# Performance work log

Measured on AMD Instinct MI355X. Metric: run time of the kernel, lower is better.

The kernel has to match this reference:

```python
import jax, jax.numpy as jnp
import numpy as np

DIM = 1024
HEADS = 16
NUM_EXPERTS = 8
TOP_K = 2
INNER = 4 * DIM
EPS = 1e-5
NEG = -1e9


def setup_inputs() -> dict:
    key = jax.random.key(0)
    ks = jax.random.split(key, 12)
    s = 0.02
    return {
        "x": jax.random.normal(ks[0], (4, 1024, DIM), dtype=jnp.float32),
        "qkv_w": jax.random.normal(ks[1], (DIM, 3 * DIM), dtype=jnp.float32) * s,
        "out_w": jax.random.normal(ks[2], (DIM, DIM), dtype=jnp.float32) * s,
        "out_b": jnp.zeros((DIM,), dtype=jnp.float32),
        "thresh": jnp.float32(-2.0),
        "ln1_g": jnp.ones((DIM,), dtype=jnp.float32),
        "ln1_b": jnp.zeros((DIM,), dtype=jnp.float32),
        "ln2_g": jnp.ones((DIM,), dtype=jnp.float32),
        "ln2_b": jnp.zeros((DIM,), dtype=jnp.float32),
        "gate_w": jax.random.normal(ks[3], (DIM, NUM_EXPERTS), dtype=jnp.float32) * s,
        "w1": jax.random.normal(ks[4], (NUM_EXPERTS, DIM, INNER), dtype=jnp.float32) * s,
        "b1": jnp.zeros((NUM_EXPERTS, INNER), dtype=jnp.float32),
        "w2": jax.random.normal(ks[5], (NUM_EXPERTS, INNER, DIM), dtype=jnp.float32) * s,
        "b2": jnp.zeros((NUM_EXPERTS, DIM), dtype=jnp.float32),
    }


def _layernorm(x, g, b):
    mu = jnp.mean(x, axis=-1, keepdims=True)
    var = jnp.mean(jnp.square(x - mu), axis=-1, keepdims=True)
    return (x - mu) * jax.lax.rsqrt(var + EPS) * g + b


def reference(x, qkv_w, out_w, out_b, thresh, ln1_g, ln1_b, ln2_g, ln2_b,
              gate_w, w1, b1, w2, b2):
    B, N, D = x.shape
    H = HEADS
    Dh = D // H
    scale = Dh ** -0.5

    # --- Sparse attention (pre-norm, eval mode: dropout off) ---
    h = _layernorm(x, ln1_g, ln1_b)
    qkv = h @ qkv_w                                   # [B,N,3D]
    q, k, v = jnp.split(qkv, 3, axis=-1)
    def heads(t):
        return t.reshape(B, N, H, Dh).transpose(0, 2, 1, 3)  # [B,H,N,Dh]
    q, k, v = heads(q), heads(k), heads(v)
    dots = jnp.einsum("bhid,bhjd->bhij", q, k) * scale
    dots = jnp.where(dots < thresh, jnp.float32(NEG), dots)  # learnable sparsity
    attn = jax.nn.softmax(dots, axis=-1)
    o = jnp.einsum("bhij,bhjd->bhid", attn, v)
    o = o.transpose(0, 2, 1, 3).reshape(B, N, D)
    x = x + o @ out_w + out_b

    # --- MoE FFN (pre-norm) ---
    h2 = _layernorm(x, ln2_g, ln2_b).reshape(-1, D)   # [T,D]
    T = h2.shape[0]
    logits = h2 @ gate_w                              # [T,E]
    probs = jax.nn.softmax(logits, axis=-1)
    aux_loss = NUM_EXPERTS * jnp.sum(probs.mean(0) * probs.sum(0))

    top_w, top_i = jax.lax.top_k(logits, TOP_K)       # [T,k]
    top_w = jax.nn.softmax(top_w, axis=-1)
    # dense combine weights: [T,E], zero for unselected experts
    combine = jnp.zeros((T, NUM_EXPERTS), dtype=h2.dtype)
    combine = combine.at[jnp.arange(T)[:, None], top_i].set(top_w)

    out = jnp.zeros_like(h2)
    for e in range(NUM_EXPERTS):
        y = jax.nn.gelu(h2 @ w1[e] + b1[e], approximate=False) @ w2[e] + b2[e]
        out = out + combine[:, e:e + 1] * y

    x = x + out.reshape(B, N, D)
    return x, aux_loss
```

## Files before the change

kernel.cpp:

```cpp
#include <hip/hip_runtime.h>
#include <math.h>

#define DIM 1024
#define THREE_DIM 3072
#define INNER 4096
#define NTOK 4096
#define NPAIR 8192
#define NEXP 8
#define MAXMB 72
#define PARTROWS (MAXMB*128)

typedef __attribute__((ext_vector_type(8))) short bf16x8;
typedef __attribute__((ext_vector_type(4))) float f32x4;
typedef long fp8x8;

__device__ __forceinline__ unsigned short f2bf(float f){
    unsigned int x = __float_as_uint(f);
    unsigned int r = x + 0x7fffu + ((x >> 16) & 1u);
    return (unsigned short)(r >> 16);
}

__device__ __forceinline__ float bf2f(unsigned short u){
    return __uint_as_float(((unsigned int)u) << 16);
}

__device__ __forceinline__ unsigned short us4c(ushort4 v, int i){
    return i == 0 ? v.x : (i == 1 ? v.y : (i == 2 ? v.z : v.w));
}

__device__ __forceinline__ unsigned int f4fp8(float a, float b, float c, float d){
    int p = __builtin_amdgcn_cvt_pk_fp8_f32(a, b, 0, false);
    p = __builtin_amdgcn_cvt_pk_fp8_f32(c, d, p, true);
    return (unsigned int)p;
}

__device__ __forceinline__ unsigned char f2fp8(float f){
    int p = __builtin_amdgcn_cvt_pk_fp8_f32(f, f, 0, false);
    return (unsigned char)(p & 0xff);
}

__device__ __forceinline__ void glds16(const void* g, void* l){
    __builtin_amdgcn_global_load_lds(
        (const __attribute__((address_space(1))) void*)g,
        (__attribute__((address_space(3))) void*)l, 16, 0, 0);
}

__device__ __forceinline__ int xcd_swz(){
    int cpx = gridDim.x >> 3;
    return (blockIdx.x & 7) * cpx + (blockIdx.x >> 3);
}

__global__ __launch_bounds__(256)
void ln_kernel(const float* __restrict__ X, const float* __restrict__ g,
               const float* __restrict__ b, float* __restrict__ outF,
               unsigned short* __restrict__ outB,
               unsigned char* __restrict__ outF8)
{
    int row = blockIdx.x;
    int t = threadIdx.x;
    const float4 v = *((const float4*)(X + (size_t)row*DIM) + t);
    float s = v.x + v.y + v.z + v.w;
    #pragma unroll
    for (int m = 1; m < 64; m <<= 1) s += __shfl_xor(s, m, 64);
    __shared__ float red[8];
    int wid = t >> 6, lane = t & 63;
    if (lane == 0) red[wid] = s;
    __syncthreads();
    float mu = (red[0]+red[1]+red[2]+red[3]) * (1.0f/DIM);
    float dx = v.x-mu, dy = v.y-mu, dz = v.z-mu, dw = v.w-mu;
    float s2 = dx*dx + dy*dy + dz*dz + dw*dw;
    #pragma unroll
    for (int m = 1; m < 64; m <<= 1) s2 += __shfl_xor(s2, m, 64);
    if (lane == 0) red[4+wid] = s2;
    __syncthreads();
    float var = (red[4]+red[5]+red[6]+red[7]) * (1.0f/DIM);
    float inv = rsqrtf(var + 1e-5f);
    const float4 gg = *((const float4*)g + t);
    const float4 bb = *((const float4*)b + t);
    float y0 = dx*inv*gg.x + bb.x;
    float y1 = dy*inv*gg.y + bb.y;
    float y2 = dz*inv*gg.z + bb.z;
    float y3 = dw*inv*gg.w + bb.w;
    if (outF){
        float4 o; o.x=y0; o.y=y1; o.z=y2; o.w=y3;
        *((float4*)(outF + (size_t)row*DIM) + t) = o;
    }
    if (outB){
        ushort4 u; u.x=f2bf(y0); u.y=f2bf(y1); u.z=f2bf(y2); u.w=f2bf(y3);
        *((ushort4*)(outB + (size_t)row*DIM) + t) = u;
    }
    if (outF8){
        *((unsigned int*)(outF8 + (size_t)row*DIM) + t) = f4fp8(y0, y1, y2, y3);
    }
}

template<int MODE>
__global__ __launch_bounds__(256)
void gemm_bf(const unsigned short* __restrict__ A,
             const unsigned short* __restrict__ BT,
             int K, int N, int gnx,
             const float* __restrict__ bias, const float* __restrict__ resid,
             unsigned short* __restrict__ outB, float* __restrict__ outF)
{
    __shared__ __align__(16) unsigned short As[128*64];
    __shared__ __align__(16) unsigned short Bs[128*64];
    int fid = xcd_swz();
    int nx = fid % gnx, my = fid / gnx;
    int m0 = my * 128, n0 = nx * 128;
    int t = threadIdx.x, lane = t & 63, wid = t >> 6;
    size_t aoff[4], boff[4];
    #pragma unroll
    for (int it = 0; it < 4; ++it){
        int chunk = it*256 + wid*64 + lane;
        int r = chunk >> 3, c16 = chunk & 7;
        int c16s = c16 ^ (r & 7);
        aoff[it] = (size_t)(m0 + r)*K + (size_t)(c16s*8);
        boff[it] = (size_t)(n0 + r)*K + (size_t)(c16s*8);
    }
    int wm = wid >> 1, wn = wid & 1;
    f32x4 acc[4][4];
    #pragma unroll
    for (int mi = 0; mi < 4; ++mi)
        #pragma unroll
        for (int ni = 0; ni < 4; ++ni)
            #pragma unroll
            for (int q = 0; q < 4; ++q) acc[mi][ni][q] = 0.f;

    for (int k0 = 0; k0 < K; k0 += 64){
        __syncthreads();
        #pragma unroll
        for (int it = 0; it < 4; ++it){
            glds16(A  + aoff[it] + k0, As + (size_t)(it*256 + wid*64)*8);
            glds16(BT + boff[it] + k0, Bs + (size_t)(it*256 + wid*64)*8);
        }
        __syncthreads();
        bf16x8 af[4][2], bg[4][2];
        #pragma unroll
        for (int mi = 0; mi < 4; ++mi){
            int row = wm*64 + mi*16 + (lane & 15);
            #pragma unroll
            for (int ks = 0; ks < 2; ++ks){
                int cg = (ks*4 + (lane >> 4)) ^ (row & 7);
                af[mi][ks] = *(const bf16x8*)&As[row*64 + cg*8];
            }
        }
        #pragma unroll
        for (int ni = 0; ni < 4; ++ni){
            int row = wn*64 + ni*16 + (lane & 15);
            #pragma unroll
            for (int ks = 0; ks < 2; ++ks){
                int cg = (ks*4 + (lane >> 4)) ^ (row & 7);
                bg[ni][ks] = *(const bf16x8*)&Bs[row*64 + cg*8];
            }
        }
        #pragma unroll
        for (int ks = 0; ks < 2; ++ks)
            #pragma unroll
            for (int mi = 0; mi < 4; ++mi)
                #pragma unroll
                for (int ni = 0; ni < 4; ++ni)
                    acc[mi][ni] = __builtin_amdgcn_mfma_f32_16x16x32_bf16(
                                      af[mi][ks], bg[ni][ks], acc[mi][ni], 0, 0, 0);
    }
    #pragma unroll
    for (int mi = 0; mi < 4; ++mi){
        #pragma unroll
        for (int ni = 0; ni < 4; ++ni){
            int ccol = n0 + wn*64 + ni*16 + (lane & 15);
            #pragma unroll
            for (int j = 0; j < 4; ++j){
                int row = m0 + wm*64 + mi*16 + (lane >> 4)*4 + j;
                float v = acc[mi][ni][j];
                if (MODE == 0){
                    outB[(size_t)row*N + ccol] = f2bf(v);
                } else {
                    outF[(size_t)row*N + ccol] =
                        v + bias[ccol] + resid[(size_t)row*N + ccol];
                }
            }
        }
    }
}

__global__ __launch_bounds__(256)
void attn4_kernel(const unsigned short* __restrict__ qkv,
                  unsigned short* __restrict__ O,
                  const float* __restrict__ threshp)
{
    __shared__ __align__(16) unsigned short Qs[64*64];
    __shared__ __align__(16) unsigned short Ks[64*64];
    __shared__ __align__(16) unsigned short Vp[8*520];
    __shared__ __align__(16) unsigned short Ps[4*1024];

    int fid = xcd_swz();
    int qt = fid & 15, hh = (fid >> 4) & 15, bb = fid >> 8;
    int t = threadIdx.x, lane = t & 63, w = t >> 6;
    int arow = lane & 15, agrp = lane >> 4;
    int qrow0 = bb*1024 + qt*64;
    float thresh = threshp[0];

    #pragma unroll
    for (int it = 0; it < 2; ++it){
        int chunk = it*256 + w*64 + lane;
        int r = chunk >> 3, c16 = chunk & 7;
        glds16(qkv + (size_t)(qrow0+r)*3072 + hh*64 + ((c16 ^ (r & 7))*8),
               Qs + (size_t)(it*256 + w*64)*8);
    }
    __syncthreads();
    bf16x8 qf[2];
    {
        int row = w*16 + arow;
        #pragma unroll
        for (int s = 0; s < 2; ++s){
            int c = (s*4 + agrp) ^ (row & 7);
            qf[s] = *(const bf16x8*)&Qs[row*64 + c*8];
        }
    }

    float m_[4], l_[4];
    f32x4 acc[4];
    #pragma unroll
    for (int j = 0; j < 4; ++j){ m_[j] = -INFINITY; l_[j] = 0.f; }
    #pragma unroll
    for (int d4 = 0; d4 < 4; ++d4)
        #pragma unroll
        for (int j = 0; j < 4; ++j) acc[d4][j] = 0.f;

    for (int kt = 0; kt < 16; ++kt){
        __syncthreads();
        int krow0 = bb*1024 + kt*64;
        #pragma unroll
        for (int it = 0; it < 2; ++it){
            int chunk = it*256 + w*64 + lane;
            int r = chunk >> 3, c16 = chunk & 7;
            glds16(qkv + (size_t)(krow0+r)*3072 + 1024 + hh*64 + ((c16 ^ (r & 7))*8),
                   Ks + (size_t)(it*256 + w*64)*8);
        }
        if (t < 128){
            int jc = t & 7, d0 = (t >> 3) * 4;
            ushort4 u[8];
            #pragma unroll
            for (int jj = 0; jj < 8; ++jj)
                u[jj] = *(const ushort4*)(qkv + (size_t)(krow0 + jc*8 + jj)*3072
                                          + 2048 + hh*64 + d0);
            #pragma unroll
            for (int i = 0; i < 4; ++i){
                ushort4 a, b;
                a.x = us4c(u[0], i); a.y = us4c(u[1], i);
                a.z = us4c(u[2], i); a.w = us4c(u[3], i);
                b.x = us4c(u[4], i); b.y = us4c(u[5], i);
                b.z = us4c(u[6], i); b.w = us4c(u[7], i);
                *(ushort4*)&Vp[jc*520 + (d0+i)*8]     = a;
                *(ushort4*)&Vp[jc*520 + (d0+i)*8 + 4] = b;
            }
        }
        __syncthreads();

        f32x4 sv[4];
        #pragma unroll
        for (int n = 0; n < 4; ++n)
            #pragma unroll
            for (int j = 0; j < 4; ++j) sv[n][j] = 0.f;
        #pragma unroll
        for (int n = 0; n < 4; ++n){
            int krow = n*16 + arow;
            #pragma unroll
            for (int s = 0; s < 2; ++s){
                int c = (s*4 + agrp) ^ (krow & 7);
                bf16x8 kf = *(const bf16x8*)&Ks[krow*64 + c*8];
                sv[n] = __builtin_amdgcn_mfma_f32_16x16x32_bf16(qf[s], kf, sv[n], 0, 0, 0);
            }
        }
        #pragma unroll
        for (int n = 0; n < 4; ++n)
            #pragma unroll
            for (int j = 0; j < 4; ++j){
                float s = sv[n][j] * 0.125f;
                sv[n][j] = (s < thresh) ? -1e9f : s;
            }
        float tmax[4], fac[4], rsum[4];
        #pragma unroll
        for (int j = 0; j < 4; ++j)
            tmax[j] = fmaxf(fmaxf(sv[0][j], sv[1][j]), fmaxf(sv[2][j], sv[3][j]));
        #pragma unroll
        for (int msk = 1; msk < 16; msk <<= 1)
            #pragma unroll
            for (int j = 0; j < 4; ++j)
                tmax[j] = fmaxf(tmax[j], __shfl_xor(tmax[j], msk, 64));
        #pragma unroll
        for (int j = 0; j < 4; ++j){
            float mn = fmaxf(m_[j], tmax[j]);
            fac[j] = __expf(m_[j] - mn);
            m_[j] = mn;
        }
        #pragma unroll
        for (int n = 0; n < 4; ++n)
            #pragma unroll
            for (int j = 0; j < 4; ++j)
                sv[n][j] = __expf(sv[n][j] - m_[j]);
        #pragma unroll
        for (int j = 0; j < 4; ++j)
            rsum[j] = sv[0][j] + sv[1][j] + sv[2][j] + sv[3][j];
        #pragma unroll
        for (int msk = 1; msk < 16; msk <<= 1)
            #pragma unroll
            for (int j = 0; j < 4; ++j)
                rsum[j] += __shfl_xor(rsum[j], msk, 64);
        #pragma unroll
        for (int j = 0; j < 4; ++j)
            l_[j] = l_[j]*fac[j] + rsum[j];
        #pragma unroll
        for (int n = 0; n < 4; ++n){
            int col = n*16 + arow;
            #pragma unroll
            for (int j = 0; j < 4; ++j){
                int r = agrp*4 + j;
                int idx = r*64 + (((col>>3) ^ (r&7)) << 3) + (col & 7);
                Ps[w*1024 + idx] = f2bf(sv[n][j]);
            }
        }
        #pragma unroll
        for (int d4 = 0; d4 < 4; ++d4)
            #pragma unroll
            for (int j = 0; j < 4; ++j) acc[d4][j] *= fac[j];
        #pragma unroll
        for (int s = 0; s < 2; ++s){
            int c = (s*4 + agrp) ^ (arow & 7);
            bf16x8 pa = *(const bf16x8*)&Ps[w*1024 + arow*64 + c*8];
            int jc = s*4 + agrp;
            #pragma unroll
            for (int d4 = 0; d4 < 4; ++d4){
                int dcol = d4*16 + arow;
                bf16x8 vb = *(const bf16x8*)&Vp[jc*520 + dcol*8];
                acc[d4] = __builtin_amdgcn_mfma_f32_16x16x32_bf16(pa, vb, acc[d4], 0, 0, 0);
            }
        }
    }
    #pragma unroll
    for (int j = 0; j < 4; ++j){
        float inv = 1.0f / l_[j];
        int row = qrow0 + w*16 + agrp*4 + j;
        #pragma unroll
        for (int d4 = 0; d4 < 4; ++d4)
            O[(size_t)row*1024 + hh*64 + d4*16 + arow] = f2bf(acc[d4][j] * inv);
    }
}

__global__ __launch_bounds__(64)
void gate_kernel(const float* __restrict__ h2, const float* __restrict__ gw,
                 float* __restrict__ probs, int* __restrict__ top_i,
                 float* __restrict__ top_w)
{
    int tk = blockIdx.x;
    int lane = threadIdx.x;
    const float* hr = h2 + (size_t)tk*DIM;
    float acc[8];
    #pragma unroll
    for (int e = 0; e < 8; ++e) acc[e] = 0.f;
    for (int d = lane; d < DIM; d += 64){
        float hv = hr[d];
        const float* grow = gw + d*8;
        #pragma unroll
        for (int e = 0; e < 8; ++e) acc[e] = fmaf(hv, grow[e], acc[e]);
    }
    #pragma unroll
    for (int m = 1; m < 64; m <<= 1)
        #pragma unroll
        for (int e = 0; e < 8; ++e) acc[e] += __shfl_xor(acc[e], m, 64);
    if (lane == 0){
        float mx = acc[0];
        #pragma unroll
        for (int e = 1; e < 8; ++e) mx = fmaxf(mx, acc[e]);
        float p[8], s = 0.f;
        #pragma unroll
        for (int e = 0; e < 8; ++e){ p[e] = __expf(acc[e]-mx); s += p[e]; }
        float invs = 1.f/s;
        #pragma unroll
        for (int e = 0; e < 8; ++e) probs[(size_t)tk*8+e] = p[e]*invs;
        int i0 = 0; float v0 = acc[0];
        #pragma unroll
        for (int e = 1; e < 8; ++e) if (acc[e] > v0){ v0 = acc[e]; i0 = e; }
        int i1 = -1; float v1 = -INFINITY;
        #pragma unroll
        for (int e = 0; e < 8; ++e) if (e != i0 && acc[e] > v1){ v1 = acc[e]; i1 = e; }
        float w0 = 1.f/(1.f + __expf(v1 - v0));
        top_i[tk*2]   = i0; top_i[tk*2+1] = i1;
        top_w[tk*2]   = w0; top_w[tk*2+1] = 1.f - w0;
    }
}

__global__ __launch_bounds__(256)
void aux_kernel(const float* __restrict__ probs, float* __restrict__ dout)
{
    int t = threadIdx.x;
    float acc[8];
    #pragma unroll
    for (int e = 0; e < 8; ++e) acc[e] = 0.f;
    for (int r = t; r < NTOK; r += 256){
        const float* pr = probs + (size_t)r*8;
        #pragma unroll
        for (int e = 0; e < 8; ++e) acc[e] += pr[e];
    }
    #pragma unroll
    for (int m = 1; m < 64; m <<= 1)
        #pragma unroll
        for (int e = 0; e < 8; ++e) acc[e] += __shfl_xor(acc[e], m, 64);
    __shared__ float red[4][8];
    int wid = t >> 6, lane = t & 63;
    if (lane == 0)
        for (int e = 0; e < 8; ++e) red[wid][e] = acc[e];
    __syncthreads();
    if (t == 0){
        float aux = 0.f;
        for (int e = 0; e < 8; ++e){
            float S = red[0][e]+red[1][e]+red[2][e]+red[3][e];
            aux += S*S;
        }
        dout[(size_t)NTOK*DIM] = aux * (8.0f/NTOK);
    }
}

__global__ __launch_bounds__(512)
void routing_kernel(const int* __restrict__ topi, int* __restrict__ perm,
                    int* __restrict__ mblk_e, int* __restrict__ tokslot)
{
    __shared__ int cnt[8];
    __shared__ int obase[8];
    int t = threadIdx.x, w = t >> 6, lane = t & 63;
    int c = 0;
    for (int i0 = 0; i0 < NPAIR; i0 += 64){
        int e = topi[i0 + lane];
        c += (e == w) ? 1 : 0;
    }
    #pragma unroll
    for (int m = 1; m < 64; m <<= 1) c += __shfl_xor(c, m, 64);
    if (lane == 0) cnt[w] = c;
    __syncthreads();
    if (t == 0){
        int mb = 0;
        for (int e = 0; e < 8; ++e){
            obase[e] = mb*128;
            int nb = (cnt[e] + 127) >> 7;
            for (int k = 0; k < nb; ++k) mblk_e[mb++] = e;
        }
        for (; mb < MAXMB; ++mb) mblk_e[mb] = -1;
    }
    __syncthreads();
    for (int i = t; i < MAXMB*128; i += 512) perm[i] = -1;
    __syncthreads();
    int base = obase[w];
    for (int i0 = 0; i0 < NPAIR; i0 += 64){
        int p = i0 + lane;
        int e = topi[p];
        bool mt = (e == w);
        unsigned long long mk = __ballot(mt);
        int rank = __popcll(mk & ((1ull << lane) - 1ull));
        if (mt){
            perm[base + rank] = p;
            tokslot[p] = base + rank;
        }
        base += __popcll(mk);
    }
}

template<int MODE>
__global__ __launch_bounds__(512, 4)
void gemm_moe8(const unsigned char* __restrict__ Abase,
               const unsigned char* __restrict__ BTbase,
               int K, int N, int lda,
               const int* __restrict__ perm, const int* __restrict__ mblk_e,
               const float* __restrict__ bias,
               unsigned char* __restrict__ actout,
               unsigned short* __restrict__ partout)
{
    const int GNX = (MODE == 2) ? (INNER/256) : (DIM/256);
    int fid = xcd_swz();
    int nx = fid % GNX;
    int rest = fid / GNX;
    int mb = rest % MAXMB;
    int kk = rest / MAXMB;
    int e = mblk_e[mb];
    if (e < 0) return;
    int kspan = (MODE == 2) ? K : (K >> 1);
    int kbeg = kk * kspan, kend = kbeg + kspan;

    __shared__ __align__(16) unsigned char As[128*64];
    __shared__ __align__(16) unsigned char Bs[256*64];
    __shared__ int permL[128];
    int t = threadIdx.x;
    if (MODE == 2 && t < 128) permL[t] = perm[mb*128 + t];
    __syncthreads();
    int lane = t & 63, wid = t >> 6;
    int wm = wid >> 2, wn = wid & 3;
    int n0 = nx * 256;
    const unsigned char* BT = BTbase + (size_t)e * (size_t)N * (size_t)K;
    size_t aoff;
    {
        int chunk = t;
        int r = chunk >> 2, c16 = chunk & 3;
        int c16s = c16 ^ (r & 3);
        size_t ar;
        if (MODE == 2){ int p = permL[r]; ar = (p >= 0) ? (size_t)(p >> 1) : 0; }
        else          { ar = (size_t)(mb*128 + r); }
        aoff = ar*(size_t)lda + (size_t)(c16s*16);
    }
    size_t boff[2];
    #pragma unroll
    for (int it = 0; it < 2; ++it){
        int chunk = it*512 + t;
        int r = chunk >> 2, c16 = chunk & 3;
        int c16s = c16 ^ (r & 3);
        boff[it] = (size_t)(n0 + r)*(size_t)K + (size_t)(c16s*16);
    }
    f32x4 acc[4][4];
    #pragma unroll
    for (int mi = 0; mi < 4; ++mi)
        #pragma unroll
        for (int ni = 0; ni < 4; ++ni)
            #pragma unroll
            for (int q = 0; q < 4; ++q) acc[mi][ni][q] = 0.f;

    for (int k0 = kbeg; k0 < kend; k0 += 64){
        __syncthreads();
        glds16(Abase + aoff + k0, As + (size_t)(wid*64 + lane)*16);
        #pragma unroll
        for (int it = 0; it < 2; ++it)
            glds16(BT + boff[it] + k0, Bs + (size_t)(it*512 + wid*64 + lane)*16);
        __syncthreads();
        #pragma unroll
        for (int ks = 0; ks < 2; ++ks){
            fp8x8 af[4], bg[4];
            #pragma unroll
            for (int mi = 0; mi < 4; ++mi){
                int row = wm*64 + mi*16 + (lane & 15);
                int o = ks*4 + (lane >> 4);
                int lc = (o >> 1) ^ (row & 3);
                af[mi] = *(const fp8x8*)&As[row*64 + lc*16 + (o & 1)*8];
            }
            #pragma unroll
            for (int ni = 0; ni < 4; ++ni){
                int row = wn*64 + ni*16 + (lane & 15);
                int o = ks*4 + (lane >> 4);
                int lc = (o >> 1) ^ (row & 3);
                bg[ni] = *(const fp8x8*)&Bs[row*64 + lc*16 + (o & 1)*8];
            }
            #pragma unroll
            for (int mi = 0; mi < 4; ++mi)
                #pragma unroll
                for (int ni = 0; ni < 4; ++ni)
                    acc[mi][ni] = __builtin_amdgcn_mfma_f32_16x16x32_fp8_fp8(
                                      af[mi], bg[ni], acc[mi][ni], 0, 0, 0);
        }
    }
    #pragma unroll
    for (int mi = 0; mi < 4; ++mi){
        #pragma unroll
        for (int ni = 0; ni < 4; ++ni){
            int ccol = n0 + wn*64 + ni*16 + (lane & 15);
            float bv = (kk == 0) ? bias[(size_t)e*N + ccol] : 0.f;
            #pragma unroll
            for (int j = 0; j < 4; ++j){
                int rloc = wm*64 + mi*16 + (lane >> 4)*4 + j;
                float v = acc[mi][ni][j];
                if (MODE == 2){
                    float gx = v + bv;
                    float z2 = gx * fmaf(gx*gx, 0.07135481283f, 1.595769122f);
                    float ex = __expf(-z2);
                    float gl = gx * __builtin_amdgcn_rcpf(1.0f + ex);
                    actout[(size_t)(mb*128 + rloc)*N + ccol] = f2fp8(gl);
                } else {
                    partout[((size_t)kk*PARTROWS + mb*128 + rloc)*N + ccol] = f2bf(v + bv);
                }
            }
        }
    }
}

__global__ __launch_bounds__(256)
void combine_kernel(const unsigned short* __restrict__ part,
                    const int* __restrict__ tokslot,
                    const float* __restrict__ topw,
                    float* __restrict__ out)
{
    int tk = blockIdx.x, t = threadIdx.x;
    int s0 = tokslot[tk*2], s1 = tokslot[tk*2+1];
    float w0 = topw[tk*2], w1 = topw[tk*2+1];
    ushort4 a0 = *((const ushort4*)(part + (size_t)s0*DIM) + t);
    ushort4 a1 = *((const ushort4*)(part + ((size_t)PARTROWS + s0)*DIM) + t);
    ushort4 b0 = *((const ushort4*)(part + (size_t)s1*DIM) + t);
    ushort4 b1 = *((const ushort4*)(part + ((size_t)PARTROWS + s1)*DIM) + t);
    float4* o4 = (float4*)(out + (size_t)tk*DIM) + t;
    float4 o = *o4;
    o.x += w0*(bf2f(a0.x) + bf2f(a1.x)) + w1*(bf2f(b0.x) + bf2f(b1.x));
    o.y += w0*(bf2f(a0.y) + bf2f(a1.y)) + w1*(bf2f(b0.y) + bf2f(b1.y));
    o.z += w0*(bf2f(a0.z) + bf2f(a1.z)) + w1*(bf2f(b0.z) + bf2f(b1.z));
    o.w += w0*(bf2f(a0.w) + bf2f(a1.w)) + w1*(bf2f(b0.w) + bf2f(b1.w));
    *o4 = o;
}

__global__ __launch_bounds__(256)
void transp_cast(const float* __restrict__ W, unsigned short* __restrict__ WT,
                 int K, int N)
{
    __shared__ float tile[32][33];
    size_t base = (size_t)blockIdx.z * (size_t)K * (size_t)N;
    const float* Wp = W + base;
    unsigned short* Tp = WT + base;
    int t = threadIdx.x;
    int r = t >> 3, c4 = (t & 7) << 2;
    int n0 = blockIdx.x << 5, k0 = blockIdx.y << 5;
    float4 v = *(const float4*)(Wp + (size_t)(k0+r)*N + n0 + c4);
    tile[r][c4+0] = v.x; tile[r][c4+1] = v.y;
    tile[r][c4+2] = v.z; tile[r][c4+3] = v.w;
    __syncthreads();
    ushort4 u;
    u.x = f2bf(tile[c4+0][r]);
    u.y = f2bf(tile[c4+1][r]);
    u.z = f2bf(tile[c4+2][r]);
    u.w = f2bf(tile[c4+3][r]);
    *(ushort4*)(Tp + (size_t)(n0+r)*K + k0 + c4) = u;
}

__global__ __launch_bounds__(256)
void transp_cast8(const float* __restrict__ W, unsigned char* __restrict__ WT,
                  int K, int N)
{
    __shared__ float tile[32][33];
    size_t base = (size_t)blockIdx.z * (size_t)K * (size_t)N;
    const float* Wp = W + base;
    unsigned char* Tp = WT + base;
    int t = threadIdx.x;
    int r = t >> 3, c4 = (t & 7) << 2;
    int n0 = blockIdx.x << 5, k0 = blockIdx.y << 5;
    float4 v = *(const float4*)(Wp + (size_t)(k0+r)*N + n0 + c4);
    tile[r][c4+0] = v.x; tile[r][c4+1] = v.y;
    tile[r][c4+2] = v.z; tile[r][c4+3] = v.w;
    __syncthreads();
    unsigned int u = f4fp8(tile[c4+0][r], tile[c4+1][r], tile[c4+2][r], tile[c4+3][r]);
    *(unsigned int*)(Tp + (size_t)(n0+r)*K + k0 + c4) = u;
}

extern "C" void kernel_launch(void* const* d_in, const int* in_sizes, int n_in,
                              void* d_out, int out_size, void* d_ws, size_t ws_size,
                              hipStream_t stream)
{
    const float* x      = (const float*)d_in[0];
    const float* qkv_w  = (const float*)d_in[1];
    const float* out_w  = (const float*)d_in[2];
    const float* out_b  = (const float*)d_in[3];
    const float* thresh = (const float*)d_in[4];
    const float* ln1_g  = (const float*)d_in[5];
    const float* ln1_b  = (const float*)d_in[6];
    const float* ln2_g  = (const float*)d_in[7];
    const float* ln2_b  = (const float*)d_in[8];
    const float* gate_w = (const float*)d_in[9];
    const float* w1     = (const float*)d_in[10];
    const float* b1     = (const float*)d_in[11];
    const float* w2     = (const float*)d_in[12];
    const float* b2     = (const float*)d_in[13];
    float* out = (float*)d_out;
    char* ws = (char*)d_ws;

    const size_t MB = (size_t)1 << 20;
    unsigned short* h1bf  = (unsigned short*)(ws);
    unsigned short* qkvbf = (unsigned short*)(ws + 8*MB);
    unsigned short* obf   = (unsigned short*)(ws + 32*MB);
    float*          h2    = (float*)(ws + 40*MB);
    unsigned char*  h2f8  = (unsigned char*)(ws + 56*MB);
    unsigned short* qwT   = (unsigned short*)(ws + 64*MB);
    unsigned short* owT   = (unsigned short*)(ws + 70*MB);
    unsigned char*  w1T8  = (unsigned char*)(ws + 72*MB);
    unsigned char*  w2T8  = (unsigned char*)(ws + 104*MB);
    unsigned char*  act8  = (unsigned char*)(ws + 136*MB);
    float* probs          = (float*)(ws + 276*MB);
    int*   top_i          = (int*)(ws + 276*MB + 131072);
    float* top_w          = (float*)(ws + 276*MB + 163840);
    int*   perm           = (int*)(ws + 276*MB + 196608);
    int*   mblk           = (int*)(ws + 276*MB + 237568);
    int*   tokslot        = (int*)(ws + 276*MB + 241664);
    unsigned short* part  = (unsigned short*)(ws + 280*MB);

    transp_cast<<<dim3(THREE_DIM/32, DIM/32, 1), 256, 0, stream>>>(qkv_w, qwT, DIM, THREE_DIM);
    transp_cast<<<dim3(DIM/32, DIM/32, 1), 256, 0, stream>>>(out_w, owT, DIM, DIM);

    ln_kernel<<<NTOK, 256, 0, stream>>>(x, ln1_g, ln1_b, nullptr, h1bf, nullptr);
    gemm_bf<0><<<(THREE_DIM/128)*(NTOK/128), 256, 0, stream>>>(
        h1bf, qwT, DIM, THREE_DIM, THREE_DIM/128, nullptr, nullptr, qkvbf, nullptr);
    attn4_kernel<<<16*16*4, 256, 0, stream>>>(qkvbf, obf, thresh);
    gemm_bf<1><<<(DIM/128)*(NTOK/128), 256, 0, stream>>>(
        obf, owT, DIM, DIM, DIM/128, out_b, x, nullptr, out);
    ln_kernel<<<NTOK, 256, 0, stream>>>(out, ln2_g, ln2_b, h2, nullptr, h2f8);
    gate_kernel<<<NTOK, 64, 0, stream>>>(h2, gate_w, probs, top_i, top_w);
    aux_kernel<<<1, 256, 0, stream>>>(probs, out);
    routing_kernel<<<1, 512, 0, stream>>>(top_i, perm, mblk, tokslot);

    transp_cast8<<<dim3(INNER/32, DIM/32, NEXP), 256, 0, stream>>>(w1, w1T8, DIM, INNER);
    transp_cast8<<<dim3(DIM/32, INNER/32, NEXP), 256, 0, stream>>>(w2, w2T8, INNER, DIM);

    gemm_moe8<2><<<(INNER/256)*MAXMB, 512, 0, stream>>>(
        h2f8, w1T8, DIM, INNER, DIM, perm, mblk, b1, act8, nullptr);
    gemm_moe8<3><<<(DIM/256)*MAXMB*2, 512, 0, stream>>>(
        act8, w2T8, INNER, DIM, INNER, perm, mblk, b2, nullptr, part);
    combine_kernel<<<NTOK, 256, 0, stream>>>(part, tokslot, top_w, out);
}
```

Measured before the change: 487.6 us.

## Double-buffer MoE FP8 GEMM loads and fuse LN2 with gating

The MoE FP8 GEMM now keeps two LDS stages and prefetches tiles two steps ahead. Explicit vmcnt waits and barriers replace the two syncthreads per k-step, and the LDS layout changes to column-chunk-major without the XOR swizzle. Separately, the second layernorm and the gate logits/top-2 routing are fused into one kernel, which removes the fp32 h2 write and its re-read. The costs are doubled LDS use, possible bank conflicts from the unswizzled layout, and fragile hand-written waitcnt logic.

```diff
diff --git a/kernel.cpp b/kernel.cpp
--- a/kernel.cpp
+++ b/kernel.cpp
@@ -52,9 +52,7 @@
 
 __global__ __launch_bounds__(256)
 void ln_kernel(const float* __restrict__ X, const float* __restrict__ g,
-               const float* __restrict__ b, float* __restrict__ outF,
-               unsigned short* __restrict__ outB,
-               unsigned char* __restrict__ outF8)
+               const float* __restrict__ b, unsigned short* __restrict__ outB)
 {
     int row = blockIdx.x;
     int t = threadIdx.x;
@@ -77,20 +75,92 @@
     float inv = rsqrtf(var + 1e-5f);
     const float4 gg = *((const float4*)g + t);
     const float4 bb = *((const float4*)b + t);
-    float y0 = dx*inv*gg.x + bb.x;
-    float y1 = dy*inv*gg.y + bb.y;
-    float y2 = dz*inv*gg.z + bb.z;
-    float y3 = dw*inv*gg.w + bb.w;
-    if (outF){
-        float4 o; o.x=y0; o.y=y1; o.z=y2; o.w=y3;
-        *((float4*)(outF + (size_t)row*DIM) + t) = o;
-    }
-    if (outB){
-        ushort4 u; u.x=f2bf(y0); u.y=f2bf(y1); u.z=f2bf(y2); u.w=f2bf(y3);
-        *((ushort4*)(outB + (size_t)row*DIM) + t) = u;
-    }
-    if (outF8){
-        *((unsigned int*)(outF8 + (size_t)row*DIM) + t) = f4fp8(y0, y1, y2, y3);
+    ushort4 u;
+    u.x = f2bf(dx*inv*gg.x + bb.x);
+    u.y = f2bf(dy*inv*gg.y + bb.y);
+    u.z = f2bf(dz*inv*gg.z + bb.z);
+    u.w = f2bf(dw*inv*gg.w + bb.w);
+    *((ushort4*)(outB + (size_t)row*DIM) + t) = u;
+}
+
+__global__ __launch_bounds__(256)
+void ln2_gate_kernel(const float* __restrict__ X, const float* __restrict__ g,
+                     const float* __restrict__ b, const float* __restrict__ gw,
+                     unsigned char* __restrict__ outF8,
+                     float* __restrict__ probs, int* __restrict__ top_i,
+                     float* __restrict__ top_w)
+{
+    int row = blockIdx.x;
+    int t = threadIdx.x;
+    const float4 v = *((const float4*)(X + (size_t)row*DIM) + t);
+    float s = v.x + v.y + v.z + v.w;
+    #pragma unroll
+    for (int m = 1; m < 64; m <<= 1) s += __shfl_xor(s, m, 64);
+    __shared__ float red[8];
+    __shared__ float red2[4][8];
+    int wid = t >> 6, lane = t & 63;
+    if (lane == 0) red[wid] = s;
+    __syncthreads();
+    float mu = (red[0]+red[1]+red[2]+red[3]) * (1.0f/DIM);
+    float dx = v.x-mu, dy = v.y-mu, dz = v.z-mu, dw = v.w-mu;
+    float s2 = dx*dx + dy*dy + dz*dz + dw*dw;
+    #pragma unroll
+    for (int m = 1; m < 64; m <<= 1) s2 += __shfl_xor(s2, m, 64);
+    if (lane == 0) red[4+wid] = s2;
+    __syncthreads();
+    float var = (red[4]+red[5]+red[6]+red[7]) * (1.0f/DIM);
+    float inv = rsqrtf(var + 1e-5f);
+    const float4 gg = *((const float4*)g + t);
+    const float4 bb = *((const float4*)b + t);
+    float y[4];
+    y[0] = dx*inv*gg.x + bb.x;
+    y[1] = dy*inv*gg.y + bb.y;
+    y[2] = dz*inv*gg.z + bb.z;
+    y[3] = dw*inv*gg.w + bb.w;
+    *((unsigned int*)(outF8 + (size_t)row*DIM) + t) = f4fp8(y[0], y[1], y[2], y[3]);
+    float ga[8];
+    #pragma unroll
+    for (int e = 0; e < 8; ++e) ga[e] = 0.f;
+    #pragma unroll
+    for (int i = 0; i < 4; ++i){
+        const float4* gr = (const float4*)(gw + (size_t)(t*4 + i)*8);
+        float4 g0 = gr[0], g1 = gr[1];
+        ga[0] = fmaf(y[i], g0.x, ga[0]); ga[1] = fmaf(y[i], g0.y, ga[1]);
+        ga[2] = fmaf(y[i], g0.z, ga[2]); ga[3] = fmaf(y[i], g0.w, ga[3]);
+        ga[4] = fmaf(y[i], g1.x, ga[4]); ga[5] = fmaf(y[i], g1.y, ga[5]);
+        ga[6] = fmaf(y[i], g1.z, ga[6]); ga[7] = fmaf(y[i], g1.w, ga[7]);
+    }
+    #pragma unroll
+    for (int m = 1; m < 64; m <<= 1)
+        #pragma unroll
+        for (int e = 0; e < 8; ++e) ga[e] += __shfl_xor(ga[e], m, 64);
+    if (lane == 0)
+        #pragma unroll
+        for (int e = 0; e < 8; ++e) red2[wid][e] = ga[e];
+    __syncthreads();
+    if (t == 0){
+        float lg[8];
+        #pragma unroll
+        for (int e = 0; e < 8; ++e)
+            lg[e] = red2[0][e] + red2[1][e] + red2[2][e] + red2[3][e];
+        float mx = lg[0];
+        #pragma unroll
+        for (int e = 1; e < 8; ++e) mx = fmaxf(mx, lg[e]);
+        float p[8], ssum = 0.f;
+        #pragma unroll
+        for (int e = 0; e < 8; ++e){ p[e] = __expf(lg[e]-mx); ssum += p[e]; }
+        float invs = 1.f/ssum;
+        #pragma unroll
+        for (int e = 0; e < 8; ++e) probs[(size_t)row*8+e] = p[e]*invs;
+        int i0 = 0; float v0 = lg[0];
+        #pragma unroll
+        for (int e = 1; e < 8; ++e) if (lg[e] > v0){ v0 = lg[e]; i0 = e; }
+        int i1 = -1; float v1 = -INFINITY;
+        #pragma unroll
+        for (int e = 0; e < 8; ++e) if (e != i0 && lg[e] > v1){ v1 = lg[e]; i1 = e; }
+        float w0 = 1.f/(1.f + __expf(v1 - v0));
+        top_i[row*2]   = i0; top_i[row*2+1] = i1;
+        top_w[row*2]   = w0; top_w[row*2+1] = 1.f - w0;
     }
 }
 
@@ -343,49 +413,6 @@
         #pragma unroll
         for (int d4 = 0; d4 < 4; ++d4)
             O[(size_t)row*1024 + hh*64 + d4*16 + arow] = f2bf(acc[d4][j] * inv);
-    }
-}
-
-__global__ __launch_bounds__(64)
-void gate_kernel(const float* __restrict__ h2, const float* __restrict__ gw,
-                 float* __restrict__ probs, int* __restrict__ top_i,
-                 float* __restrict__ top_w)
-{
-    int tk = blockIdx.x;
-    int lane = threadIdx.x;
-    const float* hr = h2 + (size_t)tk*DIM;
-    float acc[8];
-    #pragma unroll
-    for (int e = 0; e < 8; ++e) acc[e] = 0.f;
-    for (int d = lane; d < DIM; d += 64){
-        float hv = hr[d];
-        const float* grow = gw + d*8;
-        #pragma unroll
-        for (int e = 0; e < 8; ++e) acc[e] = fmaf(hv, grow[e], acc[e]);
-    }
-    #pragma unroll
-    for (int m = 1; m < 64; m <<= 1)
-        #pragma unroll
-        for (int e = 0; e < 8; ++e) acc[e] += __shfl_xor(acc[e], m, 64);
-    if (lane == 0){
-        float mx = acc[0];
-        #pragma unroll
-        for (int e = 1; e < 8; ++e) mx = fmaxf(mx, acc[e]);
-        float p[8], s = 0.f;
-        #pragma unroll
-        for (int e = 0; e < 8; ++e){ p[e] = __expf(acc[e]-mx); s += p[e]; }
-        float invs = 1.f/s;
-        #pragma unroll
-        for (int e = 0; e < 8; ++e) probs[(size_t)tk*8+e] = p[e]*invs;
-        int i0 = 0; float v0 = acc[0];
-        #pragma unroll
-        for (int e = 1; e < 8; ++e) if (acc[e] > v0){ v0 = acc[e]; i0 = e; }
-        int i1 = -1; float v1 = -INFINITY;
-        #pragma unroll
-        for (int e = 0; e < 8; ++e) if (e != i0 && acc[e] > v1){ v1 = acc[e]; i1 = e; }
-        float w0 = 1.f/(1.f + __expf(v1 - v0));
-        top_i[tk*2]   = i0; top_i[tk*2+1] = i1;
-        top_w[tk*2]   = w0; top_w[tk*2+1] = 1.f - w0;
     }
 }
 
@@ -482,10 +509,11 @@
     int e = mblk_e[mb];
     if (e < 0) return;
     int kspan = (MODE == 2) ? K : (K >> 1);
-    int kbeg = kk * kspan, kend = kbeg + kspan;
-
-    __shared__ __align__(16) unsigned char As[128*64];
-    __shared__ __align__(16) unsigned char Bs[256*64];
+    int kbeg = kk * kspan;
+    const int NT = kspan >> 6;
+
+    __shared__ __align__(16) unsigned char As[2*128*64];
+    __shared__ __align__(16) unsigned char Bs[2*256*64];
     __shared__ int permL[128];
     int t = threadIdx.x;
     if (MODE == 2 && t < 128) permL[t] = perm[mb*128 + t];
@@ -494,23 +522,18 @@
     int wm = wid >> 2, wn = wid & 3;
     int n0 = nx * 256;
     const unsigned char* BT = BTbase + (size_t)e * (size_t)N * (size_t)K;
-    size_t aoff;
+    size_t aoffA;
     {
-        int chunk = t;
-        int r = chunk >> 2, c16 = chunk & 3;
-        int c16s = c16 ^ (r & 3);
+        int r = t & 127, lc = t >> 7;
         size_t ar;
         if (MODE == 2){ int p = permL[r]; ar = (p >= 0) ? (size_t)(p >> 1) : 0; }
         else          { ar = (size_t)(mb*128 + r); }
-        aoff = ar*(size_t)lda + (size_t)(c16s*16);
-    }
-    size_t boff[2];
-    #pragma unroll
-    for (int it = 0; it < 2; ++it){
-        int chunk = it*512 + t;
-        int r = chunk >> 2, c16 = chunk & 3;
-        int c16s = c16 ^ (r & 3);
-        boff[it] = (size_t)(n0 + r)*(size_t)K + (size_t)(c16s*16);
+        aoffA = ar*(size_t)lda + (size_t)(lc*16);
+    }
+    size_t boffB0;
+    {
+        int r = t & 255, lc = t >> 8;
+        boffB0 = (size_t)(n0 + r)*(size_t)K + (size_t)(lc*16);
     }
     f32x4 acc[4][4];
     #pragma unroll
@@ -520,29 +543,34 @@
             #pragma unroll
             for (int q = 0; q < 4; ++q) acc[mi][ni][q] = 0.f;
 
-    for (int k0 = kbeg; k0 < kend; k0 += 64){
-        __syncthreads();
-        glds16(Abase + aoff + k0, As + (size_t)(wid*64 + lane)*16);
-        #pragma unroll
-        for (int it = 0; it < 2; ++it)
-            glds16(BT + boff[it] + k0, Bs + (size_t)(it*512 + wid*64 + lane)*16);
-        __syncthreads();
+    #pragma unroll
+    for (int pt = 0; pt < 2; ++pt){
+        int kq = kbeg + pt*64;
+        glds16(Abase + aoffA + kq, &As[pt*8192 + t*16]);
+        glds16(BT + boffB0 + kq,      &Bs[pt*16384 + t*16]);
+        glds16(BT + boffB0 + 32 + kq, &Bs[pt*16384 + 8192 + t*16]);
+    }
+    int cur = 0;
+    for (int kt = 0; kt < NT; ++kt){
+        if (kt < NT-1) asm volatile("s_waitcnt vmcnt(3)\ns_barrier" ::: "memory");
+        else           asm volatile("s_waitcnt vmcnt(0)\ns_barrier" ::: "memory");
+        const unsigned char* Ab = &As[cur*8192];
+        const unsigned char* Bb = &Bs[cur*16384];
+        int grp = lane >> 4;
         #pragma unroll
         for (int ks = 0; ks < 2; ++ks){
+            int lcb = ks*2 + (grp >> 1);
+            int bo  = (grp & 1)*8;
             fp8x8 af[4], bg[4];
             #pragma unroll
             for (int mi = 0; mi < 4; ++mi){
                 int row = wm*64 + mi*16 + (lane & 15);
-                int o = ks*4 + (lane >> 4);
-                int lc = (o >> 1) ^ (row & 3);
-                af[mi] = *(const fp8x8*)&As[row*64 + lc*16 + (o & 1)*8];
+                af[mi] = *(const fp8x8*)&Ab[lcb*2048 + row*16 + bo];
             }
             #pragma unroll
             for (int ni = 0; ni < 4; ++ni){
                 int row = wn*64 + ni*16 + (lane & 15);
-                int o = ks*4 + (lane >> 4);
-                int lc = (o >> 1) ^ (row & 3);
-                bg[ni] = *(const fp8x8*)&Bs[row*64 + lc*16 + (o & 1)*8];
+                bg[ni] = *(const fp8x8*)&Bb[lcb*4096 + row*16 + bo];
             }
             #pragma unroll
             for (int mi = 0; mi < 4; ++mi)
@@ -551,6 +579,14 @@
                     acc[mi][ni] = __builtin_amdgcn_mfma_f32_16x16x32_fp8_fp8(
                                       af[mi], bg[ni], acc[mi][ni], 0, 0, 0);
         }
+        asm volatile("s_barrier" ::: "memory");
+        if (kt + 2 < NT){
+            int kq = kbeg + (kt+2)*64;
+            glds16(Abase + aoffA + kq, &As[cur*8192 + t*16]);
+            glds16(BT + boffB0 + kq,      &Bs[cur*16384 + t*16]);
+            glds16(BT + boffB0 + 32 + kq, &Bs[cur*16384 + 8192 + t*16]);
+        }
+        cur ^= 1;
     }
     #pragma unroll
     for (int mi = 0; mi < 4; ++mi){
@@ -665,7 +701,6 @@
     unsigned short* h1bf  = (unsigned short*)(ws);
     unsigned short* qkvbf = (unsigned short*)(ws + 8*MB);
     unsigned short* obf   = (unsigned short*)(ws + 32*MB);
-    float*          h2    = (float*)(ws + 40*MB);
     unsigned char*  h2f8  = (unsigned char*)(ws + 56*MB);
     unsigned short* qwT   = (unsigned short*)(ws + 64*MB);
     unsigned short* owT   = (unsigned short*)(ws + 70*MB);
@@ -683,14 +718,14 @@
     transp_cast<<<dim3(THREE_DIM/32, DIM/32, 1), 256, 0, stream>>>(qkv_w, qwT, DIM, THREE_DIM);
     transp_cast<<<dim3(DIM/32, DIM/32, 1), 256, 0, stream>>>(out_w, owT, DIM, DIM);
 
-    ln_kernel<<<NTOK, 256, 0, stream>>>(x, ln1_g, ln1_b, nullptr, h1bf, nullptr);
+    ln_kernel<<<NTOK, 256, 0, stream>>>(x, ln1_g, ln1_b, h1bf);
     gemm_bf<0><<<(THREE_DIM/128)*(NTOK/128), 256, 0, stream>>>(
         h1bf, qwT, DIM, THREE_DIM, THREE_DIM/128, nullptr, nullptr, qkvbf, nullptr);
     attn4_kernel<<<16*16*4, 256, 0, stream>>>(qkvbf, obf, thresh);
     gemm_bf<1><<<(DIM/128)*(NTOK/128), 256, 0, stream>>>(
         obf, owT, DIM, DIM, DIM/128, out_b, x, nullptr, out);
-    ln_kernel<<<NTOK, 256, 0, stream>>>(out, ln2_g, ln2_b, h2, nullptr, h2f8);
-    gate_kernel<<<NTOK, 64, 0, stream>>>(h2, gate_w, probs, top_i, top_w);
+    ln2_gate_kernel<<<NTOK, 256, 0, stream>>>(out, ln2_g, ln2_b, gate_w,
+                                              h2f8, probs, top_i, top_w);
     aux_kernel<<<1, 256, 0, stream>>>(probs, out);
     routing_kernel<<<1, 512, 0, stream>>>(top_i, perm, mblk, tokslot);
 
```

Measured after the change: 487.8 us. No clear change (+0.0%).
